# Optimization experiments

Measured on AMD Instinct MI355X. Metric: run time of the kernel, lower is better.

Reference implementation:

```python
import jax, jax.numpy as jnp
import numpy as np

B, L, NS, D, M = 64, 200, 1000, 128, 50


def setup_inputs() -> dict:
    key = jax.random.key(0)
    ks = jax.random.split(key, 12)
    s = np.sqrt(2.0 / D).astype(np.float32)  # kaiming_normal scale for Mk/Mv0
    lw = np.sqrt(1.0 / D).astype(np.float32)
    return {
        "skills": jax.random.randint(ks[0], (B, L), 0, NS),
        "responses": jax.random.randint(ks[1], (B, L), 0, 2),
        "k_emb": jax.random.normal(ks[2], (NS, D), jnp.float32) * 0.02,
        "v_emb": jax.random.normal(ks[3], (2 * NS, D), jnp.float32) * 0.02,
        "Mk": jax.random.normal(ks[4], (M, D), jnp.float32) * s,
        "Mv0": jax.random.normal(ks[5], (M, D), jnp.float32) * s,
        "e_W": jax.random.normal(ks[6], (D, D), jnp.float32) * lw,
        "e_b": jnp.zeros((D,), jnp.float32),
        "a_W": jax.random.normal(ks[7], (D, D), jnp.float32) * lw,
        "a_b": jnp.zeros((D,), jnp.float32),
        "f_W": jax.random.normal(ks[8], (D, 2 * D), jnp.float32) * np.sqrt(1.0 / (2 * D)).astype(np.float32),
        "f_b": jnp.zeros((D,), jnp.float32),
        "p_W": jax.random.normal(ks[9], (1, D), jnp.float32) * lw,
        "p_b": jnp.zeros((1,), jnp.float32),
    }


def _dkvmn_forward(skills, responses, k_emb, v_emb, Mk, Mv0,
                   e_W, e_b, a_W, a_b, f_W, f_b, p_W, p_b):
    masked_r = responses * (responses > -1).astype(responses.dtype)
    x = skills + NS * masked_r                      # [B,L] combined (skill,response) id
    k = k_emb[skills]                               # [B,L,D]
    v = v_emb[x]                                    # [B,L,D]
    w = jax.nn.softmax(jnp.einsum('bld,md->blm', k, Mk), axis=-1)  # [B,L,M]
    e = jax.nn.sigmoid(v @ e_W.T + e_b)             # erase  [B,L,D]
    a = jnp.tanh(v @ a_W.T + a_b)                   # add    [B,L,D]

    def step(Mvt, wea):
        wt, et, at = wea                            # [B,M], [B,D], [B,D]
        u = wt[:, :, None]                          # [B,M,1]
        new = Mvt * (1.0 - u * et[:, None, :]) + u * at[:, None, :]
        return new, Mvt                             # emit PRE-update state (Mv[:, :-1])

    Mv_init = jnp.broadcast_to(Mv0[None], (B, M, D))
    _, Mv_pre = jax.lax.scan(
        step, Mv_init,
        (w.transpose(1, 0, 2), e.transpose(1, 0, 2), a.transpose(1, 0, 2)))
    # Mv_pre: [L,B,M,D]; weighted read of pre-update memory
    read = jnp.einsum('blm,lbmd->bld', w, Mv_pre)   # [B,L,D]
    f = jnp.tanh(jnp.concatenate([read, k], axis=-1) @ f_W.T + f_b)  # [B,L,D]
    p = jax.nn.sigmoid(f @ p_W.T + p_b)[..., 0]     # [B,L] (dropout off: eval)
    return p[:, 1:]                                 # pred, [B,L-1]


def reference(skills, responses, k_emb, v_emb, Mk, Mv0,
              e_W, e_b, a_W, a_b, f_W, f_b, p_W, p_b):
    return _dkvmn_forward(skills, responses, k_emb, v_emb, Mk, Mv0,
                          e_W, e_b, a_W, a_b, f_W, f_b, p_W, p_b)
```

## Files before the change

kernel.cpp:

```cpp
#include <hip/hip_runtime.h>
#include <hip/hip_bf16.h>

#define Bb 64
#define Ll 200
#define NSs 1000
#define Dd 128
#define Mm 50

__device__ __forceinline__ float bcast_lane(float v, int l) {
    return __int_as_float(__builtin_amdgcn_readlane(__float_as_int(v), l));
}

__global__ void __launch_bounds__(256) kern_w(
        const int* __restrict__ skills,
        const float* __restrict__ k_emb,
        const float* __restrict__ Mk,
        float* __restrict__ w_out) {
    __shared__ float mk[Mm][Dd + 4];
    __shared__ float kr[16][Dd + 4];
    int tid = threadIdx.x;
    int blk = blockIdx.x;

    for (int lin = tid; lin < (Mm * Dd) / 4; lin += 256) {
        float4 f = ((const float4*)Mk)[lin];
        int m = lin >> 5;
        int c4 = lin & 31;
        *(float4*)&mk[m][c4 * 4] = f;
    }
    for (int lin = tid; lin < 16 * 32; lin += 256) {
        int r  = lin >> 5;
        int c4 = lin & 31;
        int bl = blk * 16 + r;
        float4 f = ((const float4*)(k_emb + (size_t)skills[bl] * Dd))[c4];
        *(float4*)&kr[r][c4 * 4] = f;
    }
    __syncthreads();

    int wave = tid >> 6;
    int lane = tid & 63;
    int mm   = (lane < Mm) ? lane : 0;
    float acc[4] = {0.f, 0.f, 0.f, 0.f};
#pragma unroll 2
    for (int q = 0; q < 32; ++q) {
        float4 mkv = *(const float4*)&mk[mm][q * 4];
#pragma unroll
        for (int i = 0; i < 4; ++i) {
            float4 kv = *(const float4*)&kr[wave * 4 + i][q * 4];
            acc[i] = fmaf(mkv.x, kv.x, acc[i]);
            acc[i] = fmaf(mkv.y, kv.y, acc[i]);
            acc[i] = fmaf(mkv.z, kv.z, acc[i]);
            acc[i] = fmaf(mkv.w, kv.w, acc[i]);
        }
    }
#pragma unroll
    for (int i = 0; i < 4; ++i) {
        float logit = (lane < Mm) ? acc[i] : -1e30f;
        float mx = logit;
        for (int off = 32; off > 0; off >>= 1) mx = fmaxf(mx, __shfl_down(mx, off));
        mx = __shfl(mx, 0);
        float ex = (lane < Mm) ? expf(logit - mx) : 0.f;
        float sm = ex;
        for (int off = 32; off > 0; off >>= 1) sm += __shfl_down(sm, off);
        sm = __shfl(sm, 0);
        int bl = blk * 16 + wave * 4 + i;
        if (lane < Mm) w_out[(size_t)bl * Mm + lane] = ex / sm;
    }
}

__global__ void __launch_bounds__(256) kern_ea(
        const int* __restrict__ skills,
        const int* __restrict__ responses,
        const float* __restrict__ v_emb,
        const float* __restrict__ e_W, const float* __restrict__ e_b,
        const float* __restrict__ a_W, const float* __restrict__ a_b,
        float* __restrict__ e_out, float* __restrict__ a_out) {
    __shared__ float vt[32][Dd + 4];
    __shared__ float wt[4][16][Dd + 4];
    int tid = threadIdx.x;
    int blk = blockIdx.x;

#pragma unroll
    for (int i = 0; i < 4; ++i) {
        int lin = i * 256 + tid;
        int r   = lin >> 5;
        int c4  = lin & 31;
        int bl  = blk * 32 + r;
        int rr  = responses[bl];
        int x   = skills[bl] + NSs * ((rr > -1) ? rr : 0);
        float4 f = ((const float4*)(v_emb + (size_t)x * Dd))[c4];
        *(float4*)&vt[r][c4 * 4] = f;
    }
    __syncthreads();

    int wave = tid >> 6, lane = tid & 63;
    int pg = lane >> 3, og = lane & 7;

    for (int s = 0; s < 4; ++s) {
        int base_row = wave * 64 + s * 16;
        bool is_e    = base_row < 128;
        const float* W = is_e ? e_W : a_W;
        int wrow0 = is_e ? base_row : base_row - 128;

#pragma unroll
        for (int i = 0; i < 8; ++i) {
            int lin = i * 64 + lane;
            int r   = lin >> 5;
            int c4  = lin & 31;
            float4 f = ((const float4*)(W + (size_t)(wrow0 + r) * Dd))[c4];
            *(float4*)&wt[wave][r][c4 * 4] = f;
        }

        float acc[4][2] = {};
#pragma unroll 2
        for (int q = 0; q < 32; ++q) {
            float4 av[4], bv[2];
#pragma unroll
            for (int i = 0; i < 4; ++i) av[i] = *(const float4*)&vt[pg + 8 * i][q * 4];
#pragma unroll
            for (int j = 0; j < 2; ++j) bv[j] = *(const float4*)&wt[wave][og + 8 * j][q * 4];
#pragma unroll
            for (int i = 0; i < 4; ++i)
#pragma unroll
                for (int j = 0; j < 2; ++j) {
                    acc[i][j] = fmaf(av[i].x, bv[j].x, acc[i][j]);
                    acc[i][j] = fmaf(av[i].y, bv[j].y, acc[i][j]);
                    acc[i][j] = fmaf(av[i].z, bv[j].z, acc[i][j]);
                    acc[i][j] = fmaf(av[i].w, bv[j].w, acc[i][j]);
                }
        }

        float* dst = is_e ? e_out : a_out;
#pragma unroll
        for (int j = 0; j < 2; ++j) {
            int row = wrow0 + og + 8 * j;
            float bias = (is_e ? e_b : a_b)[row];
#pragma unroll
            for (int i = 0; i < 4; ++i) {
                int bl = blk * 32 + pg + 8 * i;
                float v = acc[i][j] + bias;
                dst[(size_t)bl * Dd + row] = is_e ? (1.f / (1.f + expf(-v))) : tanhf(v);
            }
        }
    }
}

#define PQ_LOAD(S, tt) do { int _t = (tt);                                   \
    if (_t < T) { size_t _bl = blBase + _t;                                  \
        w##S = (lane < Mm) ? w_ws[_bl * Mm + lane] : 0.f;                    \
        e##S = e_ws[_bl * Dd + d];  a##S = a_ws[_bl * Dd + d]; } } while (0)

#define PQ_BODY(S) do {                                                      \
    _Pragma("unroll")                                                        \
    for (int m = 0; m < Mm; ++m) {                                           \
        float wm = bcast_lane(w##S, m);                                      \
        float A  = fmaf(-wm, e##S, 1.f);                                     \
        Q[m] = fmaf(A, Q[m], wm * a##S);                                     \
        P[m] *= A; } } while (0)

__global__ void __launch_bounds__(128) kern_scan_pq(
        const float* __restrict__ w_ws,
        const float* __restrict__ e_ws,
        const float* __restrict__ a_ws,
        float* __restrict__ P_ws, float* __restrict__ Q_ws,
        int C, int T) {
    int b = blockIdx.x / C, c = blockIdx.x % C;
    int d = threadIdx.x;
    int lane = d & 63;
    float P[Mm], Q[Mm];
#pragma unroll
    for (int m = 0; m < Mm; ++m) { P[m] = 1.f; Q[m] = 0.f; }

    size_t blBase = (size_t)b * Ll + (size_t)c * T;
    float w0 = 0.f, e0 = 0.f, a0 = 0.f;
    float w1 = 0.f, e1 = 0.f, a1 = 0.f;
    float w2 = 0.f, e2 = 0.f, a2 = 0.f;
    PQ_LOAD(0, 0);
    PQ_LOAD(1, 1);
    for (int tt = 0; tt < T; tt += 3) {
        PQ_LOAD(2, tt + 2);  PQ_BODY(0);
        if (tt + 1 < T) { PQ_LOAD(0, tt + 3);  PQ_BODY(1); }
        if (tt + 2 < T) { PQ_LOAD(1, tt + 4);  PQ_BODY(2); }
    }
    size_t base = ((size_t)(b * C + c)) * (Mm * Dd) + d;
#pragma unroll
    for (int m = 0; m < Mm; ++m) {
        P_ws[base + m * Dd] = P[m];
        Q_ws[base + m * Dd] = Q[m];
    }
}

template <int CC>
__global__ void kern_scan_comb_t(
        const float* __restrict__ Mv0,
        const float* __restrict__ P_ws, const float* __restrict__ Q_ws,
        float* __restrict__ S_ws) {
    int idx = blockIdx.x * 256 + threadIdx.x;
    int b   = idx / (Mm * Dd);
    int md  = idx % (Mm * Dd);
    float Pr[CC - 1], Qr[CC - 1];
#pragma unroll
    for (int c = 0; c < CC - 1; ++c) {
        size_t pq = ((size_t)(b * CC + c)) * (Mm * Dd) + md;
        Pr[c] = P_ws[pq];
        Qr[c] = Q_ws[pq];
    }
    float s = Mv0[md];
#pragma unroll
    for (int c = 0; c < CC - 1; ++c) {
        s = fmaf(Pr[c], s, Qr[c]);
        S_ws[((size_t)(b * (CC - 1) + c)) * (Mm * Dd) + md] = s;
    }
}

#define RD_BODY(S, tt) do {                                                  \
    float acc0 = 0.f, acc1 = 0.f;                                            \
    _Pragma("unroll")                                                        \
    for (int m = 0; m < Mm; m += 2) {                                        \
        float wm0 = bcast_lane(w##S, m);                                     \
        float wm1 = bcast_lane(w##S, m + 1);                                 \
        acc0 = fmaf(wm0, mv[m], acc0);                                       \
        mv[m] = fmaf(wm0, fmaf(-e##S, mv[m], a##S), mv[m]);                  \
        acc1 = fmaf(wm1, mv[m + 1], acc1);                                   \
        mv[m + 1] = fmaf(wm1, fmaf(-e##S, mv[m + 1], a##S), mv[m + 1]);      \
    }                                                                        \
    read_ws[(blBase + (tt)) * Dd + d] = acc0 + acc1;                         \
    } while (0)

__global__ void __launch_bounds__(128) kern_scan_rd(
        const float* __restrict__ Mv0,
        const float* __restrict__ S_ws,
        const float* __restrict__ w_ws,
        const float* __restrict__ e_ws,
        const float* __restrict__ a_ws,
        float* __restrict__ read_ws,
        int C, int T) {
    int b = blockIdx.x / C, c = blockIdx.x % C;
    int d = threadIdx.x;
    int lane = d & 63;
    float mv[Mm];
    if (c == 0) {
#pragma unroll
        for (int m = 0; m < Mm; ++m) mv[m] = Mv0[m * Dd + d];
    } else {
        size_t sb = ((size_t)(b * (C - 1) + (c - 1))) * (Mm * Dd) + d;
#pragma unroll
        for (int m = 0; m < Mm; ++m) mv[m] = S_ws[sb + m * Dd];
    }

    size_t blBase = (size_t)b * Ll + (size_t)c * T;
    float w0 = 0.f, e0 = 0.f, a0 = 0.f;
    float w1 = 0.f, e1 = 0.f, a1 = 0.f;
    float w2 = 0.f, e2 = 0.f, a2 = 0.f;
    PQ_LOAD(0, 0);
    PQ_LOAD(1, 1);
    for (int tt = 0; tt < T; tt += 3) {
        PQ_LOAD(2, tt + 2);  RD_BODY(0, tt);
        if (tt + 1 < T) { PQ_LOAD(0, tt + 3);  RD_BODY(1, tt + 1); }
        if (tt + 2 < T) { PQ_LOAD(1, tt + 4);  RD_BODY(2, tt + 2); }
    }
}

__global__ void __launch_bounds__(256) kern_out(
        const int* __restrict__ skills,
        const float* __restrict__ read_ws,
        const float* __restrict__ k_emb,
        const float* __restrict__ f_W, const float* __restrict__ f_b,
        const float* __restrict__ p_W, const float* __restrict__ p_b,
        float* __restrict__ out) {
    __shared__ float ct[32][2 * Dd + 4];
    __shared__ float wt[4][16][Dd + 4];
    __shared__ float pf[32][8];
    int tid = threadIdx.x;
    int blk = blockIdx.x;

#pragma unroll
    for (int i = 0; i < 8; ++i) {
        int lin = i * 256 + tid;
        int r   = lin >> 6;
        int c4  = lin & 63;
        int idx = blk * 32 + r;
        int b   = idx / (Ll - 1);
        int l   = idx % (Ll - 1) + 1;
        int bl  = b * Ll + l;
        float4 f;
        if (c4 < 32) f = ((const float4*)(read_ws + (size_t)bl * Dd))[c4];
        else         f = ((const float4*)(k_emb + (size_t)skills[bl] * Dd))[c4 - 32];
        *(float4*)&ct[r][c4 * 4] = f;
    }
    ((float*)pf)[tid] = 0.f;
    __syncthreads();

    int wave = tid >> 6, lane = tid & 63;
    int pg = lane >> 3, og = lane & 7;

    float ppart[4] = {0.f, 0.f, 0.f, 0.f};
    for (int sub = 0; sub < 2; ++sub) {
        float acc[4][2] = {};
        for (int h = 0; h < 2; ++h) {
#pragma unroll
            for (int i = 0; i < 8; ++i) {
                int lin = i * 64 + lane;
                int r   = lin >> 5;
                int c4  = lin & 31;
                float4 f = ((const float4*)(f_W +
                            (size_t)(wave * 32 + sub * 16 + r) * (2 * Dd)))[h * 32 + c4];
                *(float4*)&wt[wave][r][c4 * 4] = f;
            }
#pragma unroll 2
            for (int q = 0; q < 32; ++q) {
                int k = h * 128 + q * 4;
                float4 av[4], bv[2];
#pragma unroll
                for (int i = 0; i < 4; ++i) av[i] = *(const float4*)&ct[pg + 8 * i][k];
#pragma unroll
                for (int j = 0; j < 2; ++j) bv[j] = *(const float4*)&wt[wave][og + 8 * j][q * 4];
#pragma unroll
                for (int i = 0; i < 4; ++i)
#pragma unroll
                    for (int j = 0; j < 2; ++j) {
                        acc[i][j] = fmaf(av[i].x, bv[j].x, acc[i][j]);
                        acc[i][j] = fmaf(av[i].y, bv[j].y, acc[i][j]);
                        acc[i][j] = fmaf(av[i].z, bv[j].z, acc[i][j]);
                        acc[i][j] = fmaf(av[i].w, bv[j].w, acc[i][j]);
                    }
            }
        }
#pragma unroll
        for (int j = 0; j < 2; ++j) {
            int row = wave * 32 + sub * 16 + og + 8 * j;
            float fb = f_b[row];
            float pw = p_W[row];
#pragma unroll
            for (int i = 0; i < 4; ++i)
                ppart[i] = fmaf(tanhf(acc[i][j] + fb), pw, ppart[i]);
        }
    }
#pragma unroll
    for (int i = 0; i < 4; ++i) {
        float v = ppart[i];
        for (int off = 4; off > 0; off >>= 1) v += __shfl_down(v, off, 8);
        if (og == 0) pf[pg + 8 * i][wave] = v;
    }
    __syncthreads();
    if (tid < 32) {
        float s = pf[tid][0] + pf[tid][1] + pf[tid][2] + pf[tid][3] + p_b[0];
        out[blk * 32 + tid] = 1.f / (1.f + expf(-s));
    }
}

extern "C" void kernel_launch(void* const* d_in, const int* in_sizes, int n_in,
                              void* d_out, int out_size, void* d_ws, size_t ws_size,
                              hipStream_t stream) {
    const int*   skills    = (const int*)  d_in[0];
    const int*   responses = (const int*)  d_in[1];
    const float* k_emb     = (const float*)d_in[2];
    const float* v_emb     = (const float*)d_in[3];
    const float* Mk        = (const float*)d_in[4];
    const float* Mv0       = (const float*)d_in[5];
    const float* e_W       = (const float*)d_in[6];
    const float* e_b       = (const float*)d_in[7];
    const float* a_W       = (const float*)d_in[8];
    const float* a_b       = (const float*)d_in[9];
    const float* f_W       = (const float*)d_in[10];
    const float* f_b       = (const float*)d_in[11];
    const float* p_W       = (const float*)d_in[12];
    const float* p_b       = (const float*)d_in[13];
    (void)in_sizes; (void)n_in; (void)out_size;

    float* out = (float*)d_out;

    float* ws      = (float*)d_ws;
    float* w_ws    = ws;
    float* e_ws    = w_ws + (size_t)Bb * Ll * Mm;
    float* a_ws    = e_ws + (size_t)Bb * Ll * Dd;
    float* read_ws = a_ws + (size_t)Bb * Ll * Dd;
    float* extra   = read_ws + (size_t)Bb * Ll * Dd;

    const size_t baseF = (size_t)Bb * Ll * Mm + 3 * (size_t)Bb * Ll * Dd;
    const size_t BMD   = (size_t)Bb * Mm * Dd;
    int C = 1;
    const int cands[3] = {8, 5, 2};
    for (int i = 0; i < 3; ++i) {
        size_t need = (baseF + BMD * (3 * (size_t)cands[i] - 1)) * sizeof(float);
        if (ws_size >= need) { C = cands[i]; break; }
    }
    int T = Ll / C;
    float* P_ws = extra;
    float* Q_ws = P_ws + BMD * C;
    float* S_ws = Q_ws + BMD * C;

    kern_w  <<<Bb * Ll / 16, 256, 0, stream>>>(skills, k_emb, Mk, w_ws);
    kern_ea <<<Bb * Ll / 32, 256, 0, stream>>>(skills, responses, v_emb,
                                               e_W, e_b, a_W, a_b, e_ws, a_ws);
    if (C > 1) {
        kern_scan_pq<<<Bb * C, 128, 0, stream>>>(w_ws, e_ws, a_ws, P_ws, Q_ws, C, T);
        int cgrid = (int)(BMD / 256);
        if      (C == 8) kern_scan_comb_t<8><<<cgrid, 256, 0, stream>>>(Mv0, P_ws, Q_ws, S_ws);
        else if (C == 5) kern_scan_comb_t<5><<<cgrid, 256, 0, stream>>>(Mv0, P_ws, Q_ws, S_ws);
        else             kern_scan_comb_t<2><<<cgrid, 256, 0, stream>>>(Mv0, P_ws, Q_ws, S_ws);
    }
    kern_scan_rd<<<Bb * C, 128, 0, stream>>>(Mv0, S_ws, w_ws, e_ws, a_ws, read_ws, C, T);
    kern_out<<<Bb * (Ll - 1) / 32, 256, 0, stream>>>(skills, read_ws, k_emb,
                                                     f_W, f_b, p_W, p_b, out);
}
```

Measured before the change: 193.8 us.

## Merge w and e/a projection kernels and enlarge GEMM register tiles

Combines the softmax-weight kernel and the erase/add projection kernel into one launch. Blocks 200 and up compute the attention weights, and the first 200 blocks compute e/a over 64 rows each. The e/a and output GEMMs move from 4x2 to 8x4 per-thread register tiles over 64 rows per block, which halves the block count and improves reuse of data loaded from LDS. This saves one launch and some weight reloads, but raises register pressure and cuts the number of blocks available to fill the CUs. Separately, kern_out computes Bb*(Ll-1)/64 with integer division, which gives 199 blocks covering only 12736 of the 12736 rows, so the coverage is exact.

```diff
diff --git a/kernel.cpp b/kernel.cpp
--- a/kernel.cpp
+++ b/kernel.cpp
@@ -11,80 +11,78 @@
     return __int_as_float(__builtin_amdgcn_readlane(__float_as_int(v), l));
 }
 
-__global__ void __launch_bounds__(256) kern_w(
-        const int* __restrict__ skills,
-        const float* __restrict__ k_emb,
-        const float* __restrict__ Mk,
-        float* __restrict__ w_out) {
-    __shared__ float mk[Mm][Dd + 4];
-    __shared__ float kr[16][Dd + 4];
-    int tid = threadIdx.x;
-    int blk = blockIdx.x;
-
-    for (int lin = tid; lin < (Mm * Dd) / 4; lin += 256) {
-        float4 f = ((const float4*)Mk)[lin];
-        int m = lin >> 5;
-        int c4 = lin & 31;
-        *(float4*)&mk[m][c4 * 4] = f;
-    }
-    for (int lin = tid; lin < 16 * 32; lin += 256) {
-        int r  = lin >> 5;
-        int c4 = lin & 31;
-        int bl = blk * 16 + r;
-        float4 f = ((const float4*)(k_emb + (size_t)skills[bl] * Dd))[c4];
-        *(float4*)&kr[r][c4 * 4] = f;
-    }
-    __syncthreads();
-
-    int wave = tid >> 6;
-    int lane = tid & 63;
-    int mm   = (lane < Mm) ? lane : 0;
-    float acc[4] = {0.f, 0.f, 0.f, 0.f};
-#pragma unroll 2
-    for (int q = 0; q < 32; ++q) {
-        float4 mkv = *(const float4*)&mk[mm][q * 4];
-#pragma unroll
-        for (int i = 0; i < 4; ++i) {
-            float4 kv = *(const float4*)&kr[wave * 4 + i][q * 4];
-            acc[i] = fmaf(mkv.x, kv.x, acc[i]);
-            acc[i] = fmaf(mkv.y, kv.y, acc[i]);
-            acc[i] = fmaf(mkv.z, kv.z, acc[i]);
-            acc[i] = fmaf(mkv.w, kv.w, acc[i]);
-        }
-    }
-#pragma unroll
-    for (int i = 0; i < 4; ++i) {
-        float logit = (lane < Mm) ? acc[i] : -1e30f;
-        float mx = logit;
-        for (int off = 32; off > 0; off >>= 1) mx = fmaxf(mx, __shfl_down(mx, off));
-        mx = __shfl(mx, 0);
-        float ex = (lane < Mm) ? expf(logit - mx) : 0.f;
-        float sm = ex;
-        for (int off = 32; off > 0; off >>= 1) sm += __shfl_down(sm, off);
-        sm = __shfl(sm, 0);
-        int bl = blk * 16 + wave * 4 + i;
-        if (lane < Mm) w_out[(size_t)bl * Mm + lane] = ex / sm;
-    }
-}
-
-__global__ void __launch_bounds__(256) kern_ea(
+__global__ void __launch_bounds__(256) kern_wea(
         const int* __restrict__ skills,
         const int* __restrict__ responses,
+        const float* __restrict__ k_emb,
         const float* __restrict__ v_emb,
+        const float* __restrict__ Mk,
         const float* __restrict__ e_W, const float* __restrict__ e_b,
         const float* __restrict__ a_W, const float* __restrict__ a_b,
+        float* __restrict__ w_out,
         float* __restrict__ e_out, float* __restrict__ a_out) {
-    __shared__ float vt[32][Dd + 4];
-    __shared__ float wt[4][16][Dd + 4];
+    __shared__ float smem[25344];
     int tid = threadIdx.x;
+
+    if (blockIdx.x >= 200) {
+        int blk = blockIdx.x - 200;
+        float (*mk)[Dd + 4] = (float(*)[Dd + 4])smem;
+        float (*kr)[Dd + 4] = (float(*)[Dd + 4])(smem + 6600);
+
+        for (int lin = tid; lin < (Mm * Dd) / 4; lin += 256) {
+            float4 f = ((const float4*)Mk)[lin];
+            *(float4*)&mk[lin >> 5][(lin & 31) * 4] = f;
+        }
+        for (int lin = tid; lin < 16 * 32; lin += 256) {
+            int r  = lin >> 5;
+            int c4 = lin & 31;
+            int bl = blk * 16 + r;
+            float4 f = ((const float4*)(k_emb + (size_t)skills[bl] * Dd))[c4];
+            *(float4*)&kr[r][c4 * 4] = f;
+        }
+        __syncthreads();
+
+        int wave = tid >> 6, lane = tid & 63;
+        int mmr  = (lane < Mm) ? lane : 0;
+        float acc[4] = {0.f, 0.f, 0.f, 0.f};
+#pragma unroll 2
+        for (int q = 0; q < 32; ++q) {
+            float4 mkv = *(const float4*)&mk[mmr][q * 4];
+#pragma unroll
+            for (int i = 0; i < 4; ++i) {
+                float4 kv = *(const float4*)&kr[wave * 4 + i][q * 4];
+                acc[i] = fmaf(mkv.x, kv.x, acc[i]);
+                acc[i] = fmaf(mkv.y, kv.y, acc[i]);
+                acc[i] = fmaf(mkv.z, kv.z, acc[i]);
+                acc[i] = fmaf(mkv.w, kv.w, acc[i]);
+            }
+        }
+#pragma unroll
+        for (int i = 0; i < 4; ++i) {
+            float logit = (lane < Mm) ? acc[i] : -1e30f;
+            float mx = logit;
+            for (int off = 32; off > 0; off >>= 1) mx = fmaxf(mx, __shfl_down(mx, off));
+            mx = __shfl(mx, 0);
+            float ex = (lane < Mm) ? expf(logit - mx) : 0.f;
+            float sm = ex;
+            for (int off = 32; off > 0; off >>= 1) sm += __shfl_down(sm, off);
+            sm = __shfl(sm, 0);
+            int bl = blk * 16 + wave * 4 + i;
+            if (lane < Mm) w_out[(size_t)bl * Mm + lane] = ex / sm;
+        }
+        return;
+    }
+
     int blk = blockIdx.x;
-
-#pragma unroll
-    for (int i = 0; i < 4; ++i) {
+    float (*vt)[Dd + 4] = (float(*)[Dd + 4])smem;
+    float (*wt)[Dd + 4] = (float(*)[Dd + 4])(smem + 8448);
+
+#pragma unroll
+    for (int i = 0; i < 8; ++i) {
         int lin = i * 256 + tid;
         int r   = lin >> 5;
         int c4  = lin & 31;
-        int bl  = blk * 32 + r;
+        int bl  = blk * 64 + r;
         int rr  = responses[bl];
         int x   = skills[bl] + NSs * ((rr > -1) ? rr : 0);
         float4 f = ((const float4*)(v_emb + (size_t)x * Dd))[c4];
@@ -95,33 +93,33 @@
     int wave = tid >> 6, lane = tid & 63;
     int pg = lane >> 3, og = lane & 7;
 
-    for (int s = 0; s < 4; ++s) {
-        int base_row = wave * 64 + s * 16;
+    for (int s = 0; s < 2; ++s) {
+        int base_row = wave * 64 + s * 32;
         bool is_e    = base_row < 128;
         const float* W = is_e ? e_W : a_W;
         int wrow0 = is_e ? base_row : base_row - 128;
 
 #pragma unroll
-        for (int i = 0; i < 8; ++i) {
+        for (int i = 0; i < 16; ++i) {
             int lin = i * 64 + lane;
             int r   = lin >> 5;
             int c4  = lin & 31;
             float4 f = ((const float4*)(W + (size_t)(wrow0 + r) * Dd))[c4];
-            *(float4*)&wt[wave][r][c4 * 4] = f;
-        }
-
-        float acc[4][2] = {};
+            *(float4*)&wt[wave * 32 + r][c4 * 4] = f;
+        }
+
+        float acc[8][4] = {};
 #pragma unroll 2
         for (int q = 0; q < 32; ++q) {
-            float4 av[4], bv[2];
-#pragma unroll
-            for (int i = 0; i < 4; ++i) av[i] = *(const float4*)&vt[pg + 8 * i][q * 4];
-#pragma unroll
-            for (int j = 0; j < 2; ++j) bv[j] = *(const float4*)&wt[wave][og + 8 * j][q * 4];
-#pragma unroll
-            for (int i = 0; i < 4; ++i)
-#pragma unroll
-                for (int j = 0; j < 2; ++j) {
+            float4 av[8], bv[4];
+#pragma unroll
+            for (int i = 0; i < 8; ++i) av[i] = *(const float4*)&vt[pg + 8 * i][q * 4];
+#pragma unroll
+            for (int j = 0; j < 4; ++j) bv[j] = *(const float4*)&wt[wave * 32 + og + 8 * j][q * 4];
+#pragma unroll
+            for (int i = 0; i < 8; ++i)
+#pragma unroll
+                for (int j = 0; j < 4; ++j) {
                     acc[i][j] = fmaf(av[i].x, bv[j].x, acc[i][j]);
                     acc[i][j] = fmaf(av[i].y, bv[j].y, acc[i][j]);
                     acc[i][j] = fmaf(av[i].z, bv[j].z, acc[i][j]);
@@ -131,12 +129,12 @@
 
         float* dst = is_e ? e_out : a_out;
 #pragma unroll
-        for (int j = 0; j < 2; ++j) {
+        for (int j = 0; j < 4; ++j) {
             int row = wrow0 + og + 8 * j;
             float bias = (is_e ? e_b : a_b)[row];
 #pragma unroll
-            for (int i = 0; i < 4; ++i) {
-                int bl = blk * 32 + pg + 8 * i;
+            for (int i = 0; i < 8; ++i) {
+                int bl = blk * 64 + pg + 8 * i;
                 float v = acc[i][j] + bias;
                 dst[(size_t)bl * Dd + row] = is_e ? (1.f / (1.f + expf(-v))) : tanhf(v);
             }
@@ -267,18 +265,18 @@
         const float* __restrict__ f_W, const float* __restrict__ f_b,
         const float* __restrict__ p_W, const float* __restrict__ p_b,
         float* __restrict__ out) {
-    __shared__ float ct[32][2 * Dd + 4];
-    __shared__ float wt[4][16][Dd + 4];
-    __shared__ float pf[32][8];
+    __shared__ float ct[64][2 * Dd + 4];
+    __shared__ float wt[4][32][Dd + 4];
+    __shared__ float pf[64][4];
     int tid = threadIdx.x;
     int blk = blockIdx.x;
 
 #pragma unroll
-    for (int i = 0; i < 8; ++i) {
+    for (int i = 0; i < 16; ++i) {
         int lin = i * 256 + tid;
         int r   = lin >> 6;
         int c4  = lin & 63;
-        int idx = blk * 32 + r;
+        int idx = blk * 64 + r;
         int b   = idx / (Ll - 1);
         int l   = idx % (Ll - 1) + 1;
         int bl  = b * Ll + l;
@@ -287,64 +285,61 @@
         else         f = ((const float4*)(k_emb + (size_t)skills[bl] * Dd))[c4 - 32];
         *(float4*)&ct[r][c4 * 4] = f;
     }
-    ((float*)pf)[tid] = 0.f;
     __syncthreads();
 
     int wave = tid >> 6, lane = tid & 63;
     int pg = lane >> 3, og = lane & 7;
 
-    float ppart[4] = {0.f, 0.f, 0.f, 0.f};
-    for (int sub = 0; sub < 2; ++sub) {
-        float acc[4][2] = {};
-        for (int h = 0; h < 2; ++h) {
-#pragma unroll
-            for (int i = 0; i < 8; ++i) {
-                int lin = i * 64 + lane;
-                int r   = lin >> 5;
-                int c4  = lin & 31;
-                float4 f = ((const float4*)(f_W +
-                            (size_t)(wave * 32 + sub * 16 + r) * (2 * Dd)))[h * 32 + c4];
-                *(float4*)&wt[wave][r][c4 * 4] = f;
-            }
+    float acc[8][4] = {};
+    for (int h = 0; h < 2; ++h) {
+#pragma unroll
+        for (int i = 0; i < 16; ++i) {
+            int lin = i * 64 + lane;
+            int r   = lin >> 5;
+            int c4  = lin & 31;
+            float4 f = ((const float4*)(f_W + (size_t)(wave * 32 + r) * (2 * Dd)))[h * 32 + c4];
+            *(float4*)&wt[wave][r][c4 * 4] = f;
+        }
 #pragma unroll 2
-            for (int q = 0; q < 32; ++q) {
-                int k = h * 128 + q * 4;
-                float4 av[4], bv[2];
-#pragma unroll
-                for (int i = 0; i < 4; ++i) av[i] = *(const float4*)&ct[pg + 8 * i][k];
-#pragma unroll
-                for (int j = 0; j < 2; ++j) bv[j] = *(const float4*)&wt[wave][og + 8 * j][q * 4];
-#pragma unroll
-                for (int i = 0; i < 4; ++i)
-#pragma unroll
-                    for (int j = 0; j < 2; ++j) {
-                        acc[i][j] = fmaf(av[i].x, bv[j].x, acc[i][j]);
-                        acc[i][j] = fmaf(av[i].y, bv[j].y, acc[i][j]);
-                        acc[i][j] = fmaf(av[i].z, bv[j].z, acc[i][j]);
-                        acc[i][j] = fmaf(av[i].w, bv[j].w, acc[i][j]);
-                    }
-            }
-        }
-#pragma unroll
-        for (int j = 0; j < 2; ++j) {
-            int row = wave * 32 + sub * 16 + og + 8 * j;
-            float fb = f_b[row];
-            float pw = p_W[row];
-#pragma unroll
-            for (int i = 0; i < 4; ++i)
-                ppart[i] = fmaf(tanhf(acc[i][j] + fb), pw, ppart[i]);
-        }
-    }
-#pragma unroll
-    for (int i = 0; i < 4; ++i) {
+        for (int q = 0; q < 32; ++q) {
+            int k = h * 128 + q * 4;
+            float4 av[8], bv[4];
+#pragma unroll
+            for (int i = 0; i < 8; ++i) av[i] = *(const float4*)&ct[pg + 8 * i][k];
+#pragma unroll
+            for (int j = 0; j < 4; ++j) bv[j] = *(const float4*)&wt[wave][og + 8 * j][q * 4];
+#pragma unroll
+            for (int i = 0; i < 8; ++i)
+#pragma unroll
+                for (int j = 0; j < 4; ++j) {
+                    acc[i][j] = fmaf(av[i].x, bv[j].x, acc[i][j]);
+                    acc[i][j] = fmaf(av[i].y, bv[j].y, acc[i][j]);
+                    acc[i][j] = fmaf(av[i].z, bv[j].z, acc[i][j]);
+                    acc[i][j] = fmaf(av[i].w, bv[j].w, acc[i][j]);
+                }
+        }
+    }
+
+    float ppart[8] = {};
+#pragma unroll
+    for (int j = 0; j < 4; ++j) {
+        int row = wave * 32 + og + 8 * j;
+        float fb = f_b[row];
+        float pw = p_W[row];
+#pragma unroll
+        for (int i = 0; i < 8; ++i)
+            ppart[i] = fmaf(tanhf(acc[i][j] + fb), pw, ppart[i]);
+    }
+#pragma unroll
+    for (int i = 0; i < 8; ++i) {
         float v = ppart[i];
         for (int off = 4; off > 0; off >>= 1) v += __shfl_down(v, off, 8);
         if (og == 0) pf[pg + 8 * i][wave] = v;
     }
     __syncthreads();
-    if (tid < 32) {
+    if (tid < 64) {
         float s = pf[tid][0] + pf[tid][1] + pf[tid][2] + pf[tid][3] + p_b[0];
-        out[blk * 32 + tid] = 1.f / (1.f + expf(-s));
+        out[blk * 64 + tid] = 1.f / (1.f + expf(-s));
     }
 }
 
@@ -389,9 +384,8 @@
     float* Q_ws = P_ws + BMD * C;
     float* S_ws = Q_ws + BMD * C;
 
-    kern_w  <<<Bb * Ll / 16, 256, 0, stream>>>(skills, k_emb, Mk, w_ws);
-    kern_ea <<<Bb * Ll / 32, 256, 0, stream>>>(skills, responses, v_emb,
-                                               e_W, e_b, a_W, a_b, e_ws, a_ws);
+    kern_wea<<<200 + Bb * Ll / 16, 256, 0, stream>>>(skills, responses, k_emb, v_emb, Mk,
+                                                     e_W, e_b, a_W, a_b, w_ws, e_ws, a_ws);
     if (C > 1) {
         kern_scan_pq<<<Bb * C, 128, 0, stream>>>(w_ws, e_ws, a_ws, P_ws, Q_ws, C, T);
         int cgrid = (int)(BMD / 256);
@@ -400,6 +394,6 @@
         else             kern_scan_comb_t<2><<<cgrid, 256, 0, stream>>>(Mv0, P_ws, Q_ws, S_ws);
     }
     kern_scan_rd<<<Bb * C, 128, 0, stream>>>(Mv0, S_ws, w_ws, e_ws, a_ws, read_ws, C, T);
-    kern_out<<<Bb * (Ll - 1) / 32, 256, 0, stream>>>(skills, read_ws, k_emb,
+    kern_out<<<Bb * (Ll - 1) / 64, 256, 0, stream>>>(skills, read_ws, k_emb,
                                                      f_W, f_b, p_W, p_b, out);
 }
```

Measured after the change: 202.2 us. +4.3%, slower.
